# Optimization experiments

Hardware: AMD Instinct MI355X
Metric: run time of the kernel (lower is better)

## Reference

```python
import jax, jax.numpy as jnp
import numpy as np

B, N, D, L, E = 16, 256, 128, 3, 32768  # graphs, nodes/graph, hidden_dim, num_layers, edges


def _ln(x, g, b, eps=1e-5):
    mu = jnp.mean(x, -1, keepdims=True)
    xc = x - mu
    var = jnp.mean(xc * xc, -1, keepdims=True)
    return xc * jax.lax.rsqrt(var + eps) * g + b


def setup_inputs() -> dict:
    key = jax.random.key(0)
    ks = jax.random.split(key, 16)

    def w(k, shape, fan):
        return jax.random.normal(k, shape, jnp.float32) * (fan ** -0.5)

    x = jax.random.normal(ks[0], (B * N, 1), jnp.float32)
    batch = (jnp.arange(B * N) // N).astype(jnp.int32)
    # E//B edges per graph, endpoints local to that graph (global ids = g*N + local)
    eb = jnp.repeat(jnp.arange(B, dtype=jnp.int32), E // B)
    src = jax.random.randint(ks[1], (E,), 0, N, dtype=jnp.int32)
    dst = jax.random.randint(ks[2], (E,), 0, N, dtype=jnp.int32)
    edge_index = jnp.stack([eb * N + src, eb * N + dst])
    edge_attr = jax.random.normal(ks[3], (E, 1), jnp.float32) * 0.5

    return {
        "x": x,
        "edge_index": edge_index,
        "edge_attr": edge_attr,
        "batch": batch,
        "enc_W": w(ks[4], (1, D), 1),
        "enc_b": jnp.zeros((D,), jnp.float32),
        "msg_W": w(ks[5], (L, 2 * D + 1, D), 2 * D + 1),
        "msg_b": jnp.zeros((L, D), jnp.float32),
        "msg_g": jnp.ones((L, D), jnp.float32),
        "msg_beta": jnp.zeros((L, D), jnp.float32),
        "upd_W": w(ks[6], (L, 2 * D, D), 2 * D),
        "upd_b": jnp.zeros((L, D), jnp.float32),
        "upd_g": jnp.ones((L, D), jnp.float32),
        "upd_beta": jnp.zeros((L, D), jnp.float32),
        "dec_W1": w(ks[7], (2 * D + 1, D), 2 * D + 1),
        "dec_b1": jnp.zeros((D,), jnp.float32),
        "dec_W2": w(ks[8], (D, D // 2), D),
        "dec_b2": jnp.zeros((D // 2,), jnp.float32),
        "dec_W3": w(ks[9], (D // 2, 1), D // 2),
        "dec_b3": jnp.zeros((1,), jnp.float32),
    }


def reference(x, edge_index, edge_attr, batch, enc_W, enc_b,
              msg_W, msg_b, msg_g, msg_beta,
              upd_W, upd_b, upd_g, upd_beta,
              dec_W1, dec_b1, dec_W2, dec_b2, dec_W3, dec_b3):
    n = N
    b = x.shape[0] // n
    # node encoder then dense batch: (B, N, D)
    h = (x @ enc_W + enc_b).reshape(b, n, D)

    src = edge_index[0] % n
    dst = edge_index[1] % n
    eb = batch[edge_index[0]]
    # to_dense_adj (scatter-add duplicates) then symmetrize
    adj = jnp.zeros((b, n, n), h.dtype).at[eb, src, dst].add(edge_attr[:, 0])
    adj = adj + jnp.swapaxes(adj, 1, 2)

    mask = (1.0 - jnp.eye(n, dtype=h.dtype))[None, :, :, None]  # zero self-messages
    for l in range(L):
        # cat([h_target(i), h_source(j), J]) @ W decomposed to avoid the 2D+1 concat
        Wt, Ws, wj = msg_W[l, :D], msg_W[l, D:2 * D], msg_W[l, 2 * D]
        pre = (h @ Wt)[:, :, None, :] + (h @ Ws)[:, None, :, :] \
              + adj[..., None] * wj + msg_b[l]          # (B, N, N, D)
        msgs = jax.nn.silu(_ln(pre, msg_g[l], msg_beta[l]))
        agg = jnp.sum(msgs * mask, axis=2)               # (B, N, D)
        u = jnp.concatenate([h, agg], -1) @ upd_W[l] + upd_b[l]
        h = h + jax.nn.silu(_ln(u, upd_g[l], upd_beta[l]))

    h_src = h[eb, src]
    h_dst = h[eb, dst]
    e = jnp.concatenate([h_src, h_dst, edge_attr], -1)
    e = jax.nn.silu(e @ dec_W1 + dec_b1)
    e = jax.nn.silu(e @ dec_W2 + dec_b2)
    out = jnp.tanh(e @ dec_W3 + dec_b3)
    return out[:, 0]
```

## Files before the change

kernel.cpp:

```cpp
#include <hip/hip_runtime.h>

#define NB 16
#define NN 256
#define DD 128
#define NL 3
#define NE 32768
#define BN 4096

__device__ __forceinline__ float siluf(float y) {
  return __fdividef(y, 1.0f + __expf(-y));
}

template<int CTRL>
__device__ __forceinline__ float dpp_add(float x) {
  int v = __builtin_amdgcn_update_dpp(0, __float_as_int(x), CTRL, 0xF, 0xF, true);
  return x + __int_as_float(v);
}

__device__ __forceinline__ float sum16(float x) {
  x = dpp_add<0xB1>(x);
  x = dpp_add<0x4E>(x);
  x = dpp_add<0x141>(x);
  x = dpp_add<0x140>(x);
  return x;
}

__device__ __forceinline__ float sum32(float x) {
  x = sum16(x);
  int v = __builtin_amdgcn_ds_swizzle(__float_as_int(x), 0x401F);
  return x + __int_as_float(v);
}

__device__ __forceinline__ float sum64(float x) {
  x = sum32(x);
  return x + __shfl_xor(x, 32, 64);
}


__global__ __launch_bounds__(256) void k_encode(
    const float* __restrict__ x, const float* __restrict__ W,
    const float* __restrict__ bb, float* __restrict__ h) {
  int t = blockIdx.x * 256 + threadIdx.x;
  int i = t >> 5;
  int c = (t & 31) << 2;
  float xv = x[i];
  float4 w = *(const float4*)(W + c);
  float4 bv = *(const float4*)(bb + c);
  float4 o;
  o.x = fmaf(xv, w.x, bv.x); o.y = fmaf(xv, w.y, bv.y);
  o.z = fmaf(xv, w.z, bv.z); o.w = fmaf(xv, w.w, bv.w);
  *(float4*)(h + i * DD + c) = o;
}

__global__ __launch_bounds__(256) void k_scatter(
    const int* __restrict__ ei, const float* __restrict__ ea,
    float* __restrict__ adj) {
  int e = blockIdx.x * 256 + threadIdx.x;
  int g0 = ei[e];
  int g1 = ei[NE + e];
  float v = ea[e];
  int b = g0 >> 8;
  int s = g0 & 255;
  int d = g1 & 255;
  atomicAdd(adj + (b * NN + s) * NN + d, v);
  atomicAdd(adj + (b * NN + d) * NN + s, v);
}

__global__ __launch_bounds__(64) void k_wprep(
    const float* __restrict__ msgW, float* __restrict__ wst) {
  int l = blockIdx.x;
  const float* wj = msgW + (size_t)l * (2 * DD + 1) * DD + 2 * DD * DD;
  int d0 = threadIdx.x << 1;
  float2 wv = *(const float2*)(wj + d0);
  float s1 = sum64(wv.x + wv.y);
  float s2 = sum64(fmaf(wv.x, wv.x, wv.y * wv.y));
  if (threadIdx.x == 0)
    *(float2*)(wst + 2 * l) = make_float2(s1 * 0.0078125f, s2 * 0.0078125f);
}

__global__ __launch_bounds__(256) void k_gemm2(
    const float* __restrict__ A, const float* __restrict__ W1,
    const float* __restrict__ W2, const float* __restrict__ bias1,
    const float* __restrict__ wj,
    float* __restrict__ C1, float* __restrict__ C2,
    float* __restrict__ statT, float* __restrict__ statS) {
  __shared__ float sa[8][128];
  int r = threadIdx.x >> 5;
  int c4 = (threadIdx.x & 31) << 2;
  int row0 = blockIdx.x << 3;
  ((float4*)&sa[0][0])[threadIdx.x] = ((const float4*)(A + row0 * DD))[threadIdx.x];
  __syncthreads();
  float4 a1 = {0.f, 0.f, 0.f, 0.f}, a2 = {0.f, 0.f, 0.f, 0.f};
  #pragma unroll 4
  for (int m = 0; m < DD; ++m) {
    float a = sa[r][m];
    float4 w1 = *(const float4*)(W1 + m * DD + c4);
    float4 w2 = *(const float4*)(W2 + m * DD + c4);
    a1.x = fmaf(a, w1.x, a1.x); a1.y = fmaf(a, w1.y, a1.y);
    a1.z = fmaf(a, w1.z, a1.z); a1.w = fmaf(a, w1.w, a1.w);
    a2.x = fmaf(a, w2.x, a2.x); a2.y = fmaf(a, w2.y, a2.y);
    a2.z = fmaf(a, w2.z, a2.z); a2.w = fmaf(a, w2.w, a2.w);
  }
  if (bias1) {
    float4 bv = *(const float4*)(bias1 + c4);
    a1.x += bv.x; a1.y += bv.y; a1.z += bv.z; a1.w += bv.w;
  }
  int rw = row0 + r;
  *(float4*)(C1 + rw * DD + c4) = a1;
  *(float4*)(C2 + rw * DD + c4) = a2;
  if (wj) {
    float4 wv = *(const float4*)(wj + c4);
    float s1t = sum32((a1.x + a1.y) + (a1.z + a1.w));
    float s2t = sum32(fmaf(a1.x, a1.x, a1.y * a1.y) + fmaf(a1.z, a1.z, a1.w * a1.w));
    float s3t = sum32(fmaf(a1.x, wv.x, a1.y * wv.y) + fmaf(a1.z, wv.z, a1.w * wv.w));
    float s1s = sum32((a2.x + a2.y) + (a2.z + a2.w));
    float s2s = sum32(fmaf(a2.x, a2.x, a2.y * a2.y) + fmaf(a2.z, a2.z, a2.w * a2.w));
    float s3s = sum32(fmaf(a2.x, wv.x, a2.y * wv.y) + fmaf(a2.z, wv.z, a2.w * wv.w));
    if ((threadIdx.x & 31) == 0) {
      const float inv = 0.0078125f;
      ((float4*)statT)[rw] = make_float4(s1t * inv, s2t * inv, s3t * inv, 0.f);
      ((float4*)statS)[rw] = make_float4(s1s * inv, s2s * inv, s3s * inv, 0.f);
    }
  }
}

__global__ __launch_bounds__(256) void k_ts(
    const float* __restrict__ T, const float* __restrict__ S,
    const float* __restrict__ adj,
    const float* __restrict__ statT, const float* __restrict__ statS,
    const float* __restrict__ wst, float* __restrict__ MR) {
  __shared__ float sT[64][64];
  __shared__ float sS[64][64];
  int b = blockIdx.x >> 4;
  int i0 = ((blockIdx.x >> 2) & 3) << 6;
  int j0 = (blockIdx.x & 3) << 6;
  int t = threadIdx.x;
  int ti = t >> 4, tj = t & 15;
  float acc[4][4] = {};
  int sr = t >> 2, scg = t & 3;
  const float* Trow = T + ((size_t)(b * NN + i0 + sr)) * DD + scg * 16;
  const float* Srow = S + ((size_t)(b * NN + j0 + sr)) * DD + scg * 16;
  for (int kc = 0; kc < 2; ++kc) {
    __syncthreads();
    #pragma unroll
    for (int m = 0; m < 4; ++m) {
      float4 v = *(const float4*)(Trow + kc * 64 + m * 4);
      int kk = scg * 16 + m * 4;
      sT[kk + 0][sr] = v.x; sT[kk + 1][sr] = v.y;
      sT[kk + 2][sr] = v.z; sT[kk + 3][sr] = v.w;
      float4 u = *(const float4*)(Srow + kc * 64 + m * 4);
      sS[kk + 0][sr] = u.x; sS[kk + 1][sr] = u.y;
      sS[kk + 2][sr] = u.z; sS[kk + 3][sr] = u.w;
    }
    __syncthreads();
    #pragma unroll 4
    for (int k = 0; k < 64; ++k) {
      float4 rt = *(const float4*)&sT[k][ti << 2];
      float4 rs = *(const float4*)&sS[k][tj << 2];
      acc[0][0] = fmaf(rt.x, rs.x, acc[0][0]);
      acc[0][1] = fmaf(rt.x, rs.y, acc[0][1]);
      acc[0][2] = fmaf(rt.x, rs.z, acc[0][2]);
      acc[0][3] = fmaf(rt.x, rs.w, acc[0][3]);
      acc[1][0] = fmaf(rt.y, rs.x, acc[1][0]);
      acc[1][1] = fmaf(rt.y, rs.y, acc[1][1]);
      acc[1][2] = fmaf(rt.y, rs.z, acc[1][2]);
      acc[1][3] = fmaf(rt.y, rs.w, acc[1][3]);
      acc[2][0] = fmaf(rt.z, rs.x, acc[2][0]);
      acc[2][1] = fmaf(rt.z, rs.y, acc[2][1]);
      acc[2][2] = fmaf(rt.z, rs.z, acc[2][2]);
      acc[2][3] = fmaf(rt.z, rs.w, acc[2][3]);
      acc[3][0] = fmaf(rt.w, rs.x, acc[3][0]);
      acc[3][1] = fmaf(rt.w, rs.y, acc[3][1]);
      acc[3][2] = fmaf(rt.w, rs.z, acc[3][2]);
      acc[3][3] = fmaf(rt.w, rs.w, acc[3][3]);
    }
  }
  float2 ws = *(const float2*)wst;
  float4 stT[4], stS[4];
  #pragma unroll
  for (int o = 0; o < 4; ++o) {
    stT[o] = ((const float4*)statT)[b * NN + i0 + (ti << 2) + o];
    stS[o] = ((const float4*)statS)[b * NN + j0 + (tj << 2) + o];
  }
  #pragma unroll
  for (int oi = 0; oi < 4; ++oi) {
    int row = b * NN + i0 + (ti << 2) + oi;
    float4 av = *(const float4*)(adj + (size_t)row * NN + j0 + (tj << 2));
    float R[4], NMR[4];
    #pragma unroll
    for (int oj = 0; oj < 4; ++oj) {
      float a = (oj == 0) ? av.x : (oj == 1) ? av.y : (oj == 2) ? av.z : av.w;
      float mean = stT[oi].x + stS[oj].x + a * ws.x;
      float e2 = stT[oi].y + stS[oj].y + a * a * ws.y
               + fmaf(acc[oi][oj], 0.015625f, 2.f * a * (stT[oi].z + stS[oj].z));
      float var = fmaf(-mean, mean, e2);
      float Rv = rsqrtf(var + 1e-5f);
      R[oj] = Rv;
      NMR[oj] = -mean * Rv;
    }
    float2* mrow = (float2*)MR + (size_t)row * NN + j0 + (tj << 2);
    *(float4*)(mrow)     = make_float4(R[0], NMR[0], R[1], NMR[1]);
    *(float4*)(mrow + 2) = make_float4(R[2], NMR[2], R[3], NMR[3]);
  }
}

__global__ __launch_bounds__(512, 4) void k_messages(
    const float* __restrict__ hT, const float* __restrict__ hS,
    const float* __restrict__ MR, const float* __restrict__ adj,
    const float* __restrict__ wj, const float* __restrict__ mg,
    const float* __restrict__ mbe, float* __restrict__ agg) {
  __shared__ float sh[64 * 128];
  __shared__ float sadj[8 * 256];
  __shared__ float smr[8 * 64 * 2];
  const float LN2 = 0.6931471805599453f;
  const float L2E = 1.4426950408889634f;
  int b = blockIdx.x >> 5;
  int i0 = (blockIdx.x & 31) << 3;
  int t = threadIdx.x;
  ((float4*)sadj)[t] = ((const float4*)(adj + (size_t)(b * NN + i0) * NN))[t];

  int w = t >> 6, lane = t & 63;
  int i = i0 + w, row = b * NN + i;
  int d0 = lane << 1;
  float2 tv = *(const float2*)(hT + (size_t)row * DD + d0);
  float2 wv = *(const float2*)(wj + d0);
  float2 gv = *(const float2*)(mg + d0);
  float2 bev = *(const float2*)(mbe + d0);
  float G0 = gv.x * L2E, G1 = gv.y * L2E;
  float BE0 = bev.x * L2E, BE1 = bev.y * L2E;
  float acc0 = 0.f, acc1 = 0.f;

  const float4* hsrc = (const float4*)(hS + (size_t)(b * NN) * DD);
  const float2* mrsrc = (const float2*)MR + (size_t)(b * NN + i0 + (t >> 6)) * NN + (t & 63);

  float4 p0 = hsrc[t], p1 = hsrc[t + 512], p2 = hsrc[t + 1024], p3 = hsrc[t + 1536];
  float2 pm = mrsrc[0];
  ((float4*)sh)[t] = p0; ((float4*)sh)[t + 512] = p1;
  ((float4*)sh)[t + 1024] = p2; ((float4*)sh)[t + 1536] = p3;
  ((float2*)smr)[t] = pm;
  __syncthreads();

  const float* arowb = sadj + w * NN;
  const float2* mrw = (const float2*)smr + w * 64;

  for (int c = 0; c < 4; ++c) {
    if (c < 3) {
      const float4* hn = hsrc + (c + 1) * 2048;
      p0 = hn[t]; p1 = hn[t + 512]; p2 = hn[t + 1024]; p3 = hn[t + 1536];
      pm = mrsrc[(c + 1) * 64];
    }
    const float* arow = arowb + c * 64;
    #pragma unroll 4
    for (int jj = 0; jj < 64; ++jj) {
      float2 mr = mrw[jj];
      float a = arow[jj];
      float2 hs = *(const float2*)(sh + jj * DD + d0);
      float v0 = tv.x + hs.x; v0 = fmaf(a, wv.x, v0);
      float v1 = tv.y + hs.y; v1 = fmaf(a, wv.y, v1);
      float z0 = fmaf(mr.x, v0, mr.y);
      float z1 = fmaf(mr.x, v1, mr.y);
      float yl0 = fmaf(G0, z0, BE0);
      float yl1 = fmaf(G1, z1, BE1);
      float e0 = __builtin_amdgcn_exp2f(-yl0);
      float e1 = __builtin_amdgcn_exp2f(-yl1);
      float den0 = 1.0f + e0, den1 = 1.0f + e1;
      float r = __builtin_amdgcn_rcpf(den0 * den1);
      acc0 = fmaf((yl0 * den1) * r, LN2, acc0);
      acc1 = fmaf((yl1 * den0) * r, LN2, acc1);
    }
    if ((i >> 6) == c) {
      int li = i & 63;
      float2 mr = mrw[li];
      float a = arow[li];
      float2 hs = *(const float2*)(sh + li * DD + d0);
      float v0 = tv.x + hs.x; v0 = fmaf(a, wv.x, v0);
      float v1 = tv.y + hs.y; v1 = fmaf(a, wv.y, v1);
      float z0 = fmaf(mr.x, v0, mr.y);
      float z1 = fmaf(mr.x, v1, mr.y);
      float yl0 = fmaf(G0, z0, BE0);
      float yl1 = fmaf(G1, z1, BE1);
      float e0 = __builtin_amdgcn_exp2f(-yl0);
      float e1 = __builtin_amdgcn_exp2f(-yl1);
      float den0 = 1.0f + e0, den1 = 1.0f + e1;
      float r = __builtin_amdgcn_rcpf(den0 * den1);
      acc0 = fmaf((yl0 * den1) * r, -LN2, acc0);
      acc1 = fmaf((yl1 * den0) * r, -LN2, acc1);
    }
    __syncthreads();
    if (c < 3) {
      ((float4*)sh)[t] = p0; ((float4*)sh)[t + 512] = p1;
      ((float4*)sh)[t + 1024] = p2; ((float4*)sh)[t + 1536] = p3;
      ((float2*)smr)[t] = pm;
      __syncthreads();
    }
  }
  *(float2*)(agg + (size_t)row * DD + d0) = make_float2(acc0, acc1);
}

__global__ __launch_bounds__(256) void k_update(
    float* __restrict__ h, const float* __restrict__ agg,
    const float* __restrict__ W, const float* __restrict__ ub,
    const float* __restrict__ ug, const float* __restrict__ ube) {
  __shared__ float scat[8][256];
  int r = threadIdx.x >> 5;
  int c4 = (threadIdx.x & 31) << 2;
  int row0 = blockIdx.x << 3;
  {
    int t = threadIdx.x;
    float4 v = ((const float4*)(h + row0 * DD))[t];
    int f = t << 2; int rr = f >> 7; int mm = f & 127;
    *(float4*)&scat[rr][mm] = v;
    float4 va = ((const float4*)(agg + row0 * DD))[t];
    *(float4*)&scat[rr][DD + mm] = va;
  }
  __syncthreads();
  float4 acc = *(const float4*)(ub + c4);
  #pragma unroll 4
  for (int m = 0; m < 2 * DD; ++m) {
    float a = scat[r][m];
    float4 wv = *(const float4*)(W + m * DD + c4);
    acc.x = fmaf(a, wv.x, acc.x);
    acc.y = fmaf(a, wv.y, acc.y);
    acc.z = fmaf(a, wv.z, acc.z);
    acc.w = fmaf(a, wv.w, acc.w);
  }
  float s1 = sum32((acc.x + acc.y) + (acc.z + acc.w));
  float s2 = sum32(fmaf(acc.x, acc.x, acc.y * acc.y) + fmaf(acc.z, acc.z, acc.w * acc.w));
  float mean = s1 * 0.0078125f;
  float var = fmaf(-mean, mean, s2 * 0.0078125f);
  float rstd = rsqrtf(var + 1e-5f);
  float4 g  = *(const float4*)(ug + c4);
  float4 be = *(const float4*)(ube + c4);
  float4 ho = *(const float4*)&scat[r][c4];
  float4 o;
  o.x = ho.x + siluf(fmaf((acc.x - mean) * rstd, g.x, be.x));
  o.y = ho.y + siluf(fmaf((acc.y - mean) * rstd, g.y, be.y));
  o.z = ho.z + siluf(fmaf((acc.z - mean) * rstd, g.z, be.z));
  o.w = ho.w + siluf(fmaf((acc.w - mean) * rstd, g.w, be.w));
  *(float4*)(h + (row0 + r) * DD + c4) = o;
}

__global__ __launch_bounds__(256, 2) void k_decoder(
    const int* __restrict__ ei, const float* __restrict__ ea,
    const float* __restrict__ P, const float* __restrict__ Q,
    const float* __restrict__ w1e, const float* __restrict__ b1,
    const float* __restrict__ W2, const float* __restrict__ b2,
    const float* __restrict__ W3, const float* __restrict__ b3,
    float* __restrict__ out) {
  __shared__ float sS[64][132];
  int t = threadIdx.x;
  {
    int e = t >> 2, qq = t & 3;
    int eg = (blockIdx.x << 6) + e;
    int g0 = ei[eg], g1 = ei[NE + eg];
    float av = ea[eg];
    const float4* p4 = (const float4*)(P + (size_t)g0 * DD + qq * 32);
    const float4* q4 = (const float4*)(Q + (size_t)g1 * DD + qq * 32);
    const float4* w4 = (const float4*)(w1e + qq * 32);
    const float4* b4 = (const float4*)(b1 + qq * 32);
    #pragma unroll
    for (int m = 0; m < 8; ++m) {
      float4 p = p4[m], qv = q4[m], wv = w4[m], bv = b4[m];
      float4 sv;
      sv.x = siluf(fmaf(av, wv.x, (p.x + qv.x) + bv.x));
      sv.y = siluf(fmaf(av, wv.y, (p.y + qv.y) + bv.y));
      sv.z = siluf(fmaf(av, wv.z, (p.z + qv.z) + bv.z));
      sv.w = siluf(fmaf(av, wv.w, (p.w + qv.w) + bv.w));
      *(float4*)&sS[e][(qq << 5) + (m << 2)] = sv;
    }
  }
  __syncthreads();
  int ti = t >> 4, tj = t & 15;
  float4 acc[4] = {{0.f,0.f,0.f,0.f},{0.f,0.f,0.f,0.f},{0.f,0.f,0.f,0.f},{0.f,0.f,0.f,0.f}};
  const float4* W2g = (const float4*)W2;
  #pragma unroll 4
  for (int k4 = 0; k4 < 32; ++k4) {
    float4 sv[4], wv[4];
    #pragma unroll
    for (int r = 0; r < 4; ++r)
      sv[r] = *(const float4*)&sS[(ti << 2) + r][k4 << 2];
    #pragma unroll
    for (int kk = 0; kk < 4; ++kk)
      wv[kk] = W2g[(((k4 << 2) + kk) << 4) + tj];
    #pragma unroll
    for (int r = 0; r < 4; ++r) {
      acc[r].x = fmaf(sv[r].x, wv[0].x, acc[r].x);
      acc[r].y = fmaf(sv[r].x, wv[0].y, acc[r].y);
      acc[r].z = fmaf(sv[r].x, wv[0].z, acc[r].z);
      acc[r].w = fmaf(sv[r].x, wv[0].w, acc[r].w);
      acc[r].x = fmaf(sv[r].y, wv[1].x, acc[r].x);
      acc[r].y = fmaf(sv[r].y, wv[1].y, acc[r].y);
      acc[r].z = fmaf(sv[r].y, wv[1].z, acc[r].z);
      acc[r].w = fmaf(sv[r].y, wv[1].w, acc[r].w);
      acc[r].x = fmaf(sv[r].z, wv[2].x, acc[r].x);
      acc[r].y = fmaf(sv[r].z, wv[2].y, acc[r].y);
      acc[r].z = fmaf(sv[r].z, wv[2].z, acc[r].z);
      acc[r].w = fmaf(sv[r].z, wv[2].w, acc[r].w);
      acc[r].x = fmaf(sv[r].w, wv[3].x, acc[r].x);
      acc[r].y = fmaf(sv[r].w, wv[3].y, acc[r].y);
      acc[r].z = fmaf(sv[r].w, wv[3].z, acc[r].z);
      acc[r].w = fmaf(sv[r].w, wv[3].w, acc[r].w);
    }
  }
  float4 b2v = *(const float4*)(b2 + (tj << 2));
  float4 w3v = *(const float4*)(W3 + (tj << 2));
  float b3v = b3[0];
  #pragma unroll
  for (int r = 0; r < 4; ++r) {
    float part = siluf(acc[r].x + b2v.x) * w3v.x;
    part = fmaf(siluf(acc[r].y + b2v.y), w3v.y, part);
    part = fmaf(siluf(acc[r].z + b2v.z), w3v.z, part);
    part = fmaf(siluf(acc[r].w + b2v.w), w3v.w, part);
    part = sum16(part);
    if (tj == 0)
      out[(blockIdx.x << 6) + (ti << 2) + r] = tanhf(part + b3v);
  }
}

extern "C" void kernel_launch(void* const* d_in, const int* in_sizes, int n_in,
                              void* d_out, int out_size, void* d_ws, size_t ws_size,
                              hipStream_t stream) {
  const float* x     = (const float*)d_in[0];
  const int*   ei    = (const int*)  d_in[1];
  const float* ea    = (const float*)d_in[2];
  const float* encW  = (const float*)d_in[4];
  const float* encb  = (const float*)d_in[5];
  const float* msgW  = (const float*)d_in[6];
  const float* msgb  = (const float*)d_in[7];
  const float* msgg  = (const float*)d_in[8];
  const float* msgbe = (const float*)d_in[9];
  const float* updW  = (const float*)d_in[10];
  const float* updb  = (const float*)d_in[11];
  const float* updg  = (const float*)d_in[12];
  const float* updbe = (const float*)d_in[13];
  const float* dW1   = (const float*)d_in[14];
  const float* db1   = (const float*)d_in[15];
  const float* dW2   = (const float*)d_in[16];
  const float* db2   = (const float*)d_in[17];
  const float* dW3   = (const float*)d_in[18];
  const float* db3   = (const float*)d_in[19];
  float* out = (float*)d_out;

  float* h     = (float*)d_ws;
  float* adj   = h     + BN * DD;
  float* hT    = adj   + NB * NN * NN;
  float* hS    = hT    + BN * DD;
  float* agg   = hS    + BN * DD;
  float* W2T   = agg   + BN * DD;
  float* statT = W2T   + 64 * DD;
  float* statS = statT + BN * 4;
  float* wst   = statS + BN * 4;
  float* MR    = wst   + 8;

  hipMemsetAsync(adj, 0, (size_t)NB * NN * NN * sizeof(float), stream);
  k_encode<<<512, 256, 0, stream>>>(x, encW, encb, h);
  k_scatter<<<NE / 256, 256, 0, stream>>>(ei, ea, adj);
  k_wprep<<<NL, 64, 0, stream>>>(msgW, wst);

  for (int l = 0; l < NL; ++l) {
    const float* Wl = msgW + (size_t)l * (2 * DD + 1) * DD;
    const float* wjl = Wl + 2 * DD * DD;
    k_gemm2<<<BN / 8, 256, 0, stream>>>(h, Wl, Wl + DD * DD, msgb + l * DD, wjl,
                                        hT, hS, statT, statS);
    k_ts<<<256, 256, 0, stream>>>(hT, hS, adj, statT, statS, wst + 2 * l, MR);
    k_messages<<<512, 512, 0, stream>>>(hT, hS, MR, adj, wjl,
        msgg + l * DD, msgbe + l * DD, agg);
    k_update<<<BN / 8, 256, 0, stream>>>(h, agg, updW + (size_t)l * 2 * DD * DD,
        updb + l * DD, updg + l * DD, updbe + l * DD);
  }

  k_gemm2<<<BN / 8, 256, 0, stream>>>(h, dW1, dW1 + DD * DD, nullptr, nullptr,
                                      hT, hS, statT, statS);
  k_decoder<<<NE / 64, 256, 0, stream>>>(ei, ea, hT, hS, dW1 + 2 * DD * DD, db1,
      dW2, db2, dW3, db3, out);
}
```

Before: 328.7 us.

## Split message rows across j-halves and pack adj into per-pair stats

```diff
diff --git a/kernel.cpp b/kernel.cpp
--- a/kernel.cpp
+++ b/kernel.cpp
@@ -128,7 +128,7 @@
     const float* __restrict__ T, const float* __restrict__ S,
     const float* __restrict__ adj,
     const float* __restrict__ statT, const float* __restrict__ statS,
-    const float* __restrict__ wst, float* __restrict__ MR) {
+    const float* __restrict__ wst, float* __restrict__ MR4) {
   __shared__ float sT[64][64];
   __shared__ float sS[64][64];
   int b = blockIdx.x >> 4;
@@ -186,7 +186,7 @@
   for (int oi = 0; oi < 4; ++oi) {
     int row = b * NN + i0 + (ti << 2) + oi;
     float4 av = *(const float4*)(adj + (size_t)row * NN + j0 + (tj << 2));
-    float R[4], NMR[4];
+    float4* m4row = (float4*)MR4 + (size_t)row * NN + j0 + (tj << 2);
     #pragma unroll
     for (int oj = 0; oj < 4; ++oj) {
       float a = (oj == 0) ? av.x : (oj == 1) ? av.y : (oj == 2) ? av.z : av.w;
@@ -195,32 +195,26 @@
                + fmaf(acc[oi][oj], 0.015625f, 2.f * a * (stT[oi].z + stS[oj].z));
       float var = fmaf(-mean, mean, e2);
       float Rv = rsqrtf(var + 1e-5f);
-      R[oj] = Rv;
-      NMR[oj] = -mean * Rv;
-    }
-    float2* mrow = (float2*)MR + (size_t)row * NN + j0 + (tj << 2);
-    *(float4*)(mrow)     = make_float4(R[0], NMR[0], R[1], NMR[1]);
-    *(float4*)(mrow + 2) = make_float4(R[2], NMR[2], R[3], NMR[3]);
-  }
-}
-
-__global__ __launch_bounds__(512, 4) void k_messages(
+      m4row[oj] = make_float4(Rv, -mean * Rv, a, 0.f);
+    }
+  }
+}
+
+__global__ __launch_bounds__(512, 6) void k_messages(
     const float* __restrict__ hT, const float* __restrict__ hS,
-    const float* __restrict__ MR, const float* __restrict__ adj,
-    const float* __restrict__ wj, const float* __restrict__ mg,
-    const float* __restrict__ mbe, float* __restrict__ agg) {
+    const float* __restrict__ MR4, const float* __restrict__ wj,
+    const float* __restrict__ mg, const float* __restrict__ mbe,
+    float* __restrict__ agg) {
   __shared__ float sh[64 * 128];
-  __shared__ float sadj[8 * 256];
-  __shared__ float smr[8 * 64 * 2];
+  __shared__ float4 smr[256];
   const float LN2 = 0.6931471805599453f;
   const float L2E = 1.4426950408889634f;
-  int b = blockIdx.x >> 5;
-  int i0 = (blockIdx.x & 31) << 3;
+  int b = blockIdx.x >> 6;
+  int i0 = (blockIdx.x & 63) << 2;
   int t = threadIdx.x;
-  ((float4*)sadj)[t] = ((const float4*)(adj + (size_t)(b * NN + i0) * NN))[t];
-
   int w = t >> 6, lane = t & 63;
-  int i = i0 + w, row = b * NN + i;
+  int il = w >> 1, jh = w & 1, jb = jh << 5;
+  int i = i0 + il, row = b * NN + i;
   int d0 = lane << 1;
   float2 tv = *(const float2*)(hT + (size_t)row * DD + d0);
   float2 wv = *(const float2*)(wj + d0);
@@ -231,70 +225,76 @@
   float acc0 = 0.f, acc1 = 0.f;
 
   const float4* hsrc = (const float4*)(hS + (size_t)(b * NN) * DD);
-  const float2* mrsrc = (const float2*)MR + (size_t)(b * NN + i0 + (t >> 6)) * NN + (t & 63);
+  int ml = t >> 6, mj = t & 63;
+  const float4* msrc = (const float4*)MR4 + (size_t)(b * NN + i0 + ml) * NN + mj;
 
   float4 p0 = hsrc[t], p1 = hsrc[t + 512], p2 = hsrc[t + 1024], p3 = hsrc[t + 1536];
-  float2 pm = mrsrc[0];
+  float4 pm;
+  if (t < 256) pm = msrc[0];
   ((float4*)sh)[t] = p0; ((float4*)sh)[t + 512] = p1;
   ((float4*)sh)[t + 1024] = p2; ((float4*)sh)[t + 1536] = p3;
-  ((float2*)smr)[t] = pm;
+  if (t < 256) smr[t] = pm;
   __syncthreads();
 
-  const float* arowb = sadj + w * NN;
-  const float2* mrw = (const float2*)smr + w * 64;
+  const float4* mrw = smr + (il << 6) + jb;
 
   for (int c = 0; c < 4; ++c) {
     if (c < 3) {
       const float4* hn = hsrc + (c + 1) * 2048;
       p0 = hn[t]; p1 = hn[t + 512]; p2 = hn[t + 1024]; p3 = hn[t + 1536];
-      pm = mrsrc[(c + 1) * 64];
-    }
-    const float* arow = arowb + c * 64;
+      if (t < 256) pm = msrc[(c + 1) * 64];
+    }
     #pragma unroll 4
-    for (int jj = 0; jj < 64; ++jj) {
-      float2 mr = mrw[jj];
-      float a = arow[jj];
-      float2 hs = *(const float2*)(sh + jj * DD + d0);
-      float v0 = tv.x + hs.x; v0 = fmaf(a, wv.x, v0);
-      float v1 = tv.y + hs.y; v1 = fmaf(a, wv.y, v1);
-      float z0 = fmaf(mr.x, v0, mr.y);
-      float z1 = fmaf(mr.x, v1, mr.y);
+    for (int jj = 0; jj < 32; ++jj) {
+      float4 m4 = mrw[jj];
+      float2 hs = *(const float2*)(sh + ((jb + jj) << 7) + d0);
+      float v0 = tv.x + hs.x; v0 = fmaf(m4.z, wv.x, v0);
+      float v1 = tv.y + hs.y; v1 = fmaf(m4.z, wv.y, v1);
+      float z0 = fmaf(m4.x, v0, m4.y);
+      float z1 = fmaf(m4.x, v1, m4.y);
       float yl0 = fmaf(G0, z0, BE0);
       float yl1 = fmaf(G1, z1, BE1);
       float e0 = __builtin_amdgcn_exp2f(-yl0);
       float e1 = __builtin_amdgcn_exp2f(-yl1);
       float den0 = 1.0f + e0, den1 = 1.0f + e1;
       float r = __builtin_amdgcn_rcpf(den0 * den1);
-      acc0 = fmaf((yl0 * den1) * r, LN2, acc0);
-      acc1 = fmaf((yl1 * den0) * r, LN2, acc1);
-    }
-    if ((i >> 6) == c) {
-      int li = i & 63;
-      float2 mr = mrw[li];
-      float a = arow[li];
-      float2 hs = *(const float2*)(sh + li * DD + d0);
-      float v0 = tv.x + hs.x; v0 = fmaf(a, wv.x, v0);
-      float v1 = tv.y + hs.y; v1 = fmaf(a, wv.y, v1);
-      float z0 = fmaf(mr.x, v0, mr.y);
-      float z1 = fmaf(mr.x, v1, mr.y);
+      acc0 = fmaf(yl0 * den1, r, acc0);
+      acc1 = fmaf(yl1 * den0, r, acc1);
+    }
+    if ((i >> 6) == c && ((i >> 5) & 1) == jh) {
+      int li = i & 31;
+      float4 m4 = mrw[li];
+      float2 hs = *(const float2*)(sh + ((jb + li) << 7) + d0);
+      float v0 = tv.x + hs.x; v0 = fmaf(m4.z, wv.x, v0);
+      float v1 = tv.y + hs.y; v1 = fmaf(m4.z, wv.y, v1);
+      float z0 = fmaf(m4.x, v0, m4.y);
+      float z1 = fmaf(m4.x, v1, m4.y);
       float yl0 = fmaf(G0, z0, BE0);
       float yl1 = fmaf(G1, z1, BE1);
       float e0 = __builtin_amdgcn_exp2f(-yl0);
       float e1 = __builtin_amdgcn_exp2f(-yl1);
       float den0 = 1.0f + e0, den1 = 1.0f + e1;
       float r = __builtin_amdgcn_rcpf(den0 * den1);
-      acc0 = fmaf((yl0 * den1) * r, -LN2, acc0);
-      acc1 = fmaf((yl1 * den0) * r, -LN2, acc1);
+      acc0 = fmaf(yl0 * den1, -r, acc0);
+      acc1 = fmaf(yl1 * den0, -r, acc1);
     }
     __syncthreads();
     if (c < 3) {
       ((float4*)sh)[t] = p0; ((float4*)sh)[t + 512] = p1;
       ((float4*)sh)[t + 1024] = p2; ((float4*)sh)[t + 1536] = p3;
-      ((float2*)smr)[t] = pm;
+      if (t < 256) smr[t] = pm;
       __syncthreads();
     }
   }
-  *(float2*)(agg + (size_t)row * DD + d0) = make_float2(acc0, acc1);
+  if (jh == 1)
+    ((float2*)smr)[(il << 6) + lane] = make_float2(acc0, acc1);
+  __syncthreads();
+  if (jh == 0) {
+    float2 o = ((float2*)smr)[(il << 6) + lane];
+    acc0 += o.x; acc1 += o.y;
+    *(float2*)(agg + (size_t)row * DD + d0) =
+        make_float2(acc0 * LN2, acc1 * LN2);
+  }
 }
 
 __global__ __launch_bounds__(256) void k_update(
@@ -446,11 +446,10 @@
   float* hT    = adj   + NB * NN * NN;
   float* hS    = hT    + BN * DD;
   float* agg   = hS    + BN * DD;
-  float* W2T   = agg   + BN * DD;
-  float* statT = W2T   + 64 * DD;
+  float* statT = agg   + BN * DD;
   float* statS = statT + BN * 4;
   float* wst   = statS + BN * 4;
-  float* MR    = wst   + 8;
+  float* MR4   = wst   + 8;
 
   hipMemsetAsync(adj, 0, (size_t)NB * NN * NN * sizeof(float), stream);
   k_encode<<<512, 256, 0, stream>>>(x, encW, encb, h);
@@ -462,8 +461,8 @@
     const float* wjl = Wl + 2 * DD * DD;
     k_gemm2<<<BN / 8, 256, 0, stream>>>(h, Wl, Wl + DD * DD, msgb + l * DD, wjl,
                                         hT, hS, statT, statS);
-    k_ts<<<256, 256, 0, stream>>>(hT, hS, adj, statT, statS, wst + 2 * l, MR);
-    k_messages<<<512, 512, 0, stream>>>(hT, hS, MR, adj, wjl,
+    k_ts<<<256, 256, 0, stream>>>(hT, hS, adj, statT, statS, wst + 2 * l, MR4);
+    k_messages<<<1024, 512, 0, stream>>>(hT, hS, MR4, wjl,
         msgg + l * DD, msgbe + l * DD, agg);
     k_update<<<BN / 8, 256, 0, stream>>>(h, agg, updW + (size_t)l * 2 * DD * DD,
         updb + l * DD, updg + l * DD, updbe + l * DD);
```

Result: no change. 327.2 us (-0.5%).
